# Optimization experiments

Hardware: AMD Instinct MI355X
Metric: run time of the kernel (lower is better)

Reference implementation:

```python
import jax, jax.numpy as jnp
import numpy as np
import math

EMBED = 768
HEADS = 12
DK = EMBED // HEADS
FFN = 3072
NQ = 8
B, S = 4, 2048


def _layernorm(x, g, b, eps=1e-5):
    mu = jnp.mean(x, axis=-1, keepdims=True)
    var = jnp.var(x, axis=-1, keepdims=True)
    return (x - mu) * jax.lax.rsqrt(var + eps) * g + b


def setup_inputs() -> dict:
    key = jax.random.key(0)
    ks = jax.random.split(key, 16)
    std = 0.02
    inp = {
        "x": jax.random.normal(ks[0], (B, S, EMBED), dtype=jnp.float32),
        "mask": jnp.ones((B, S), dtype=jnp.int32),
        # attention projections (torch Linear: W [out, in])
        "wq": jax.random.normal(ks[1], (EMBED, EMBED), jnp.float32) * std,
        "bq": jnp.zeros((EMBED,), jnp.float32),
        "wk": jax.random.normal(ks[2], (EMBED, EMBED), jnp.float32) * std,
        "bk": jnp.zeros((EMBED,), jnp.float32),
        "wv": jax.random.normal(ks[3], (EMBED, EMBED), jnp.float32) * std,
        "bv": jnp.zeros((EMBED,), jnp.float32),
        "wo": jax.random.normal(ks[4], (EMBED, EMBED), jnp.float32) * std,
        "bo": jnp.zeros((EMBED,), jnp.float32),
        # layernorms
        "g1": jnp.ones((EMBED,), jnp.float32),
        "be1": jnp.zeros((EMBED,), jnp.float32),
        "g2": jnp.ones((EMBED,), jnp.float32),
        "be2": jnp.zeros((EMBED,), jnp.float32),
        # quantum FFN: trainable RY angles + two linears
        "theta": jax.random.normal(ks[5], (NQ,), jnp.float32) * 0.1,
        "w1": jax.random.normal(ks[6], (FFN, NQ), jnp.float32) * std,
        "b1": jnp.zeros((FFN,), jnp.float32),
        "w2": jax.random.normal(ks[7], (EMBED, FFN), jnp.float32) * std,
        "b2": jnp.zeros((EMBED,), jnp.float32),
    }
    return inp


def _block(x, mask, wq, bq, wk, bk, wv, bv, wo, bo, g1, be1, g2, be2,
           theta, w1, b1, w2, b2):
    b, s, _ = x.shape
    # --- multi-head attention (dropout = identity at eval) ---
    q = (x @ wq.T + bq).reshape(b, s, HEADS, DK)
    k = (x @ wk.T + bk).reshape(b, s, HEADS, DK)
    v = (x @ wv.T + bv).reshape(b, s, HEADS, DK)
    scores = jnp.einsum("bqhd,bkhd->bhqk", q, k) / math.sqrt(DK)
    scores = jnp.where(mask[:, None, None, :] == 0, -1e9, scores)
    attn = jax.nn.softmax(scores, axis=-1)
    ctx = jnp.einsum("bhqk,bkhd->bqhd", attn, v).reshape(b, s, EMBED)
    attn_out = ctx @ wo.T + bo
    x = _layernorm(x + attn_out, g1, be1)
    # --- quantum FFN: RY(x_i) then RY(theta_i) on |0>, <Z> = cos(x_i+theta_i)
    # (product state, no entanglement -> exact closed form, fully batched)
    meas = jnp.cos(x[..., :NQ] + theta)            # [b, s, NQ]
    h = jax.nn.relu(meas @ w1.T + b1)              # [b, s, FFN]
    ffn_out = h @ w2.T + b2                        # [b, s, EMBED]
    return _layernorm(x + ffn_out, g2, be2)


def reference(x, mask, wq, bq, wk, bk, wv, bv, wo, bo, g1, be1, g2, be2,
              theta, w1, b1, w2, b2):
    return _block(x, mask, wq, bq, wk, bk, wv, bv, wo, bo,
                  g1, be1, g2, be2, theta, w1, b1, w2, b2)
```

## Files before the change

### kernel.cpp

```cpp
#include <hip/hip_runtime.h>
#include <hip/hip_bf16.h>


typedef __bf16 bf16_t;
typedef bf16_t bf16x4 __attribute__((ext_vector_type(4)));
typedef bf16_t bf16x8 __attribute__((ext_vector_type(8)));
typedef float floatx4 __attribute__((ext_vector_type(4)));

#define LOG2E 1.44269504088896f

__device__ __forceinline__ void gload16(const bf16_t* g, bf16_t* l) {
    __builtin_amdgcn_global_load_lds(
        (const __attribute__((address_space(1))) unsigned int*)g,
        (__attribute__((address_space(3))) unsigned int*)l,
        16, 0, 0);
}

__global__ __launch_bounds__(256)
void prep(const float* __restrict__ x,
          const float* __restrict__ wq, const float* __restrict__ wk,
          const float* __restrict__ wv, const float* __restrict__ wo,
          const float* __restrict__ w2,
          const float* __restrict__ bq, const float* __restrict__ bk,
          const float* __restrict__ bv,
          bf16_t* __restrict__ xb, bf16_t* __restrict__ wqkv,
          bf16_t* __restrict__ wob, bf16_t* __restrict__ w2b,
          float* __restrict__ bqkv)
{
    const int seg = blockIdx.y;
    const int idx = blockIdx.x * 256 + threadIdx.x;
    if (seg == 0) {
        if (idx >= 1572864) return;
        const float4 f = ((const float4*)x)[idx];
        bf16x4 o = {(bf16_t)f.x, (bf16_t)f.y, (bf16_t)f.z, (bf16_t)f.w};
        ((bf16x4*)xb)[idx] = o;
    } else if (seg == 1) {
        if (idx >= 442368) return;
        const int e = idx * 4;
        const float4 f = (e < 589824) ? ((const float4*)wq)[idx]
                       : (e < 1179648) ? ((const float4*)wk)[idx - 147456]
                                       : ((const float4*)wv)[idx - 294912];
        bf16x4 o = {(bf16_t)f.x, (bf16_t)f.y, (bf16_t)f.z, (bf16_t)f.w};
        ((bf16x4*)wqkv)[idx] = o;
    } else if (seg == 2) {
        if (idx >= 147456) return;
        const float4 f = ((const float4*)wo)[idx];
        bf16x4 o = {(bf16_t)f.x, (bf16_t)f.y, (bf16_t)f.z, (bf16_t)f.w};
        ((bf16x4*)wob)[idx] = o;
    } else if (seg == 3) {
        if (idx >= 589824) return;
        const float4 f = ((const float4*)w2)[idx];
        bf16x4 o = {(bf16_t)f.x, (bf16_t)f.y, (bf16_t)f.z, (bf16_t)f.w};
        ((bf16x4*)w2b)[idx] = o;
    } else {
        if (idx >= 576) return;
        const int e = idx * 4;
        const float4 f = (e < 768) ? ((const float4*)bq)[idx]
                       : (e < 1536) ? ((const float4*)bk)[idx - 192]
                                    : ((const float4*)bv)[idx - 384];
        ((float4*)bqkv)[idx] = f;
    }
}

template<typename TC>
__global__ __launch_bounds__(256)
void gemm_bb(const bf16_t* __restrict__ A, const bf16_t* __restrict__ W,
             const float* __restrict__ bias, TC* __restrict__ C,
             int kPer, int lda, int ldw, int ldc, int splitStride)
{
    __shared__ __align__(16) bf16_t As[4096];
    __shared__ __align__(16) bf16_t Bs[4096];
    const int tid  = threadIdx.x;
    const int wave = tid >> 6;
    const int lane = tid & 63;
    const int wm = (wave >> 1) * 64;
    const int wn = (wave & 1) * 64;
    const int bm = blockIdx.y * 128;
    const int bn = blockIdx.x * 128;
    const int fr = lane & 15;
    const int fk = (lane >> 4) * 8;

    const int kBeg = blockIdx.z * kPer;
    const int kEnd = kBeg + kPer;
    C += (size_t)blockIdx.z * splitStride;

    const int srow = tid >> 2;
    const int scol = (tid & 3) * 8;
    bf16_t* lA = &As[tid * 8];
    bf16_t* lB = &Bs[tid * 8];

    floatx4 acc[4][4] = {};

    for (int k0 = kBeg; k0 < kEnd; k0 += 32) {
        const bf16_t* ga = A + (size_t)(bm + srow) * lda + k0 + scol;
        const bf16_t* gb = W + (size_t)(bn + srow) * ldw + k0 + scol;
        gload16(ga,                     lA);
        gload16(ga + (size_t)64 * lda,  lA + 2048);
        gload16(gb,                     lB);
        gload16(gb + (size_t)64 * ldw,  lB + 2048);
        __syncthreads();

        bf16x8 fa[4], fb[4];
        #pragma unroll
        for (int i = 0; i < 4; ++i) {
            fa[i] = *(const bf16x8*)&As[(wm + i * 16 + fr) * 32 + fk];
            fb[i] = *(const bf16x8*)&Bs[(wn + i * 16 + fr) * 32 + fk];
        }
        #pragma unroll
        for (int mi = 0; mi < 4; ++mi)
            #pragma unroll
            for (int ni = 0; ni < 4; ++ni)
                acc[mi][ni] = __builtin_amdgcn_mfma_f32_16x16x32_bf16(
                    fa[mi], fb[ni], acc[mi][ni], 0, 0, 0);
        __syncthreads();
    }

    const int fg = (lane >> 4) * 4;
    const bool addb = (blockIdx.z == 0);
    #pragma unroll
    for (int mi = 0; mi < 4; ++mi) {
        #pragma unroll
        for (int ni = 0; ni < 4; ++ni) {
            const int col = bn + wn + ni * 16 + fr;
            const float bv = addb ? bias[col] : 0.f;
            #pragma unroll
            for (int r = 0; r < 4; ++r) {
                const int row = bm + wm + mi * 16 + fg + r;
                C[(size_t)row * ldc + col] = (TC)(acc[mi][ni][r] + bv);
            }
        }
    }
}

__global__ __launch_bounds__(256)
void attn_mfma(const bf16_t* __restrict__ qkv, const int* __restrict__ mask,
               bf16_t* __restrict__ ctx)
{
    __shared__ bf16_t Ks[64][72];
    __shared__ bf16_t Vt[80][72];
    __shared__ float  mb_s[64];
    __shared__ bf16_t Pl[4][32][72];

    const int bh = blockIdx.y;
    const int b = bh / 12, h = bh % 12;
    const int tid  = threadIdx.x;
    const int wave = tid >> 6;
    const int lane = tid & 63;
    const int g    = lane >> 4;
    const int fr   = lane & 15;
    const int qbase = blockIdx.x * 128 + wave * 32;

    for (int idx = tid; idx < 16 * 72; idx += 256) {
        const int rr = idx / 72, cc = idx % 72;
        Vt[64 + rr][cc] = (bf16_t)(rr == 0 ? 1.f : 0.f);
    }

    bf16x8 qf[2][2];
    #pragma unroll
    for (int qt = 0; qt < 2; ++qt)
        #pragma unroll
        for (int s = 0; s < 2; ++s) {
            const size_t tok = (size_t)(b * 2048 + qbase + qt * 16 + fr);
            qf[qt][s] = *(const bf16x8*)(qkv + tok * 2304 + h * 64 + s * 32 + g * 8);
            #pragma unroll
            for (int j = 0; j < 8; ++j)
                qf[qt][s][j] = (bf16_t)((float)qf[qt][s][j] * 0.125f);
        }

    floatx4 o[2][4] = {};
    floatx4 oe[2] = {};

    const int skey = tid & 63;
    const int sgrp = tid >> 6;

    for (int kt = 0; kt < 32; ++kt) {
        __syncthreads();
        {
            const size_t ktok = (size_t)(b * 2048 + kt * 64 + skey) * 2304 + h * 64;
            const bf16x8 k0 = *(const bf16x8*)(qkv + ktok + 768 + sgrp * 16);
            const bf16x8 k1 = *(const bf16x8*)(qkv + ktok + 768 + sgrp * 16 + 8);
            *(bf16x8*)&Ks[skey][sgrp * 16]     = k0;
            *(bf16x8*)&Ks[skey][sgrp * 16 + 8] = k1;
            const bf16x8 v0 = *(const bf16x8*)(qkv + ktok + 1536 + sgrp * 16);
            const bf16x8 v1 = *(const bf16x8*)(qkv + ktok + 1536 + sgrp * 16 + 8);
            #pragma unroll
            for (int j = 0; j < 8; ++j) {
                Vt[sgrp * 16 + j][skey]     = v0[j];
                Vt[sgrp * 16 + 8 + j][skey] = v1[j];
            }
            if (tid < 64)
                mb_s[tid] = (mask[b * 2048 + kt * 64 + tid] == 0) ? -1e9f : 0.f;
        }
        __syncthreads();

        floatx4 st_[2][4] = {};
        #pragma unroll
        for (int s = 0; s < 2; ++s) {
            bf16x8 kf[4];
            #pragma unroll
            for (int ct = 0; ct < 4; ++ct)
                kf[ct] = *(const bf16x8*)&Ks[ct * 16 + fr][s * 32 + g * 8];
            #pragma unroll
            for (int qt = 0; qt < 2; ++qt)
                #pragma unroll
                for (int ct = 0; ct < 4; ++ct)
                    st_[qt][ct] = __builtin_amdgcn_mfma_f32_16x16x32_bf16(
                        kf[ct], qf[qt][s], st_[qt][ct], 0, 0, 0);
        }

        #pragma unroll
        for (int qt = 0; qt < 2; ++qt) {
            #pragma unroll
            for (int ct = 0; ct < 4; ++ct) {
                const float4 mb4 = *(const float4*)&mb_s[ct * 16 + g * 4];
                const float mbr[4] = { mb4.x, mb4.y, mb4.z, mb4.w };
                bf16x4 pw;
                #pragma unroll
                for (int r = 0; r < 4; ++r)
                    pw[r] = (bf16_t)__builtin_amdgcn_exp2f(
                        fmaf(st_[qt][ct][r], LOG2E, mbr[r]));
                *(bf16x4*)&Pl[wave][qt * 16 + fr][ct * 16 + g * 4] = pw;
            }
        }

        #pragma unroll
        for (int st2 = 0; st2 < 2; ++st2) {
            bf16x8 pf[2];
            #pragma unroll
            for (int qt = 0; qt < 2; ++qt)
                pf[qt] = *(const bf16x8*)&Pl[wave][qt * 16 + fr][st2 * 32 + g * 8];
            #pragma unroll
            for (int dt = 0; dt < 4; ++dt) {
                const bf16x8 vf = *(const bf16x8*)&Vt[dt * 16 + fr][st2 * 32 + g * 8];
                #pragma unroll
                for (int qt = 0; qt < 2; ++qt)
                    o[qt][dt] = __builtin_amdgcn_mfma_f32_16x16x32_bf16(
                        pf[qt], vf, o[qt][dt], 0, 0, 0);
            }
            const bf16x8 vo = *(const bf16x8*)&Vt[64 + fr][st2 * 32 + g * 8];
            #pragma unroll
            for (int qt = 0; qt < 2; ++qt)
                oe[qt] = __builtin_amdgcn_mfma_f32_16x16x32_bf16(
                    pf[qt], vo, oe[qt], 0, 0, 0);
        }
    }

    #pragma unroll
    for (int qt = 0; qt < 2; ++qt) {
        float inv[4];
        #pragma unroll
        for (int r = 0; r < 4; ++r) {
            const float lv = __shfl(oe[qt][r], (lane & 48), 64);
            inv[r] = 1.f / lv;
        }
        #pragma unroll
        for (int dt = 0; dt < 4; ++dt)
            #pragma unroll
            for (int r = 0; r < 4; ++r) {
                const size_t row = (size_t)(b * 2048 + qbase + qt * 16 + g * 4 + r);
                ctx[row * 768 + h * 64 + dt * 16 + fr] = (bf16_t)(o[qt][dt][r] * inv[r]);
            }
    }
}

__global__ __launch_bounds__(256)
void ln_fuse(const float* __restrict__ xin, const float* __restrict__ proj,
             const float* __restrict__ proj2,
             const float* __restrict__ g, const float* __restrict__ be,
             float* __restrict__ out,
             const float* __restrict__ theta, float* __restrict__ meas)
{
    const int row = blockIdx.x;
    const int tid = threadIdx.x;
    const size_t base = (size_t)row * 768;
    float v0 = xin[base + tid]       + proj[base + tid];
    float v1 = xin[base + tid + 256] + proj[base + tid + 256];
    float v2 = xin[base + tid + 512] + proj[base + tid + 512];
    if (proj2 != nullptr) {
        v0 += proj2[base + tid];
        v1 += proj2[base + tid + 256];
        v2 += proj2[base + tid + 512];
    }
    float s1 = v0 + v1 + v2;
    float s2 = v0*v0 + v1*v1 + v2*v2;
    #pragma unroll
    for (int mk = 32; mk >= 1; mk >>= 1) {
        s1 += __shfl_xor(s1, mk, 64);
        s2 += __shfl_xor(s2, mk, 64);
    }
    __shared__ float w1s[4], w2s[4];
    const int wave = tid >> 6;
    if ((tid & 63) == 0) { w1s[wave] = s1; w2s[wave] = s2; }
    __syncthreads();
    const float tot1 = w1s[0] + w1s[1] + w1s[2] + w1s[3];
    const float tot2 = w2s[0] + w2s[1] + w2s[2] + w2s[3];
    const float mu   = tot1 * (1.f / 768.f);
    const float var  = tot2 * (1.f / 768.f) - mu * mu;
    const float rinv = rsqrtf(var + 1e-5f);
    const float y0 = (v0 - mu) * rinv * g[tid] + be[tid];
    out[base + tid]       = y0;
    out[base + tid + 256] = (v1 - mu) * rinv * g[tid + 256] + be[tid + 256];
    out[base + tid + 512] = (v2 - mu) * rinv * g[tid + 512] + be[tid + 512];
    if (meas != nullptr && tid < 8)
        meas[row * 8 + tid] = cosf(y0 + theta[tid]);
}

__global__ __launch_bounds__(256)
void ffn1(const float* __restrict__ meas, const float* __restrict__ w1,
          const float* __restrict__ b1, bf16_t* __restrict__ h)
{
    const int row = blockIdx.x;
    __shared__ float ms[8];
    if (threadIdx.x < 8) ms[threadIdx.x] = meas[row * 8 + threadIdx.x];
    __syncthreads();
    #pragma unroll
    for (int i = 0; i < 12; ++i) {
        const int f = threadIdx.x + i * 256;
        const float4 wa = *(const float4*)(w1 + f * 8);
        const float4 wb = *(const float4*)(w1 + f * 8 + 4);
        float v = b1[f];
        v += ms[0]*wa.x + ms[1]*wa.y + ms[2]*wa.z + ms[3]*wa.w;
        v += ms[4]*wb.x + ms[5]*wb.y + ms[6]*wb.z + ms[7]*wb.w;
        h[(size_t)row * 3072 + f] = (bf16_t)fmaxf(v, 0.f);
    }
}

extern "C" void kernel_launch(void* const* d_in, const int* in_sizes, int n_in,
                              void* d_out, int out_size, void* d_ws, size_t ws_size,
                              hipStream_t stream)
{
    const float* x     = (const float*)d_in[0];
    const int*   mask  = (const int*)d_in[1];
    const float* wq    = (const float*)d_in[2];
    const float* bq    = (const float*)d_in[3];
    const float* wk    = (const float*)d_in[4];
    const float* bk    = (const float*)d_in[5];
    const float* wv    = (const float*)d_in[6];
    const float* bv    = (const float*)d_in[7];
    const float* wo    = (const float*)d_in[8];
    const float* bo    = (const float*)d_in[9];
    const float* g1    = (const float*)d_in[10];
    const float* be1   = (const float*)d_in[11];
    const float* g2    = (const float*)d_in[12];
    const float* be2   = (const float*)d_in[13];
    const float* theta = (const float*)d_in[14];
    const float* w1    = (const float*)d_in[15];
    const float* b1    = (const float*)d_in[16];
    const float* w2    = (const float*)d_in[17];
    const float* b2    = (const float*)d_in[18];
    float* out = (float*)d_out;

    char* ws = (char*)d_ws;
    bf16_t* qkv    = (bf16_t*)(ws + 0);
    bf16_t* ctx    = (bf16_t*)(ws + 37748736);
    float*  attnp  = (float*)(ws + 50331648);
    float*  y      = (float*)(ws + 100663296);
    float*  meas   = (float*)(ws + 125829120);
    bf16_t* xb     = (bf16_t*)(ws + 126091264);
    bf16_t* wqkv   = (bf16_t*)(ws + 138674176);
    bf16_t* wob    = (bf16_t*)(ws + 142213120);
    bf16_t* w2b    = (bf16_t*)(ws + 143392768);
    float*  bqkv   = (float*)(ws + 148111360);
    float*  ffnp   = (float*)(ws + 0);
    bf16_t* h      = (bf16_t*)(ws + 50331648);

    const dim3 blk(256);

    prep<<<dim3(6144, 5), blk, 0, stream>>>(x, wq, wk, wv, wo, w2, bq, bk, bv,
                                            xb, wqkv, wob, w2b, bqkv);

    gemm_bb<bf16_t><<<dim3(18, 64, 1), blk, 0, stream>>>(
        xb, wqkv, bqkv, qkv, 768, 768, 768, 2304, 0);

    attn_mfma<<<dim3(16, 48), blk, 0, stream>>>(qkv, mask, ctx);

    gemm_bb<float><<<dim3(6, 64, 2), blk, 0, stream>>>(
        ctx, wob, bo, attnp, 384, 768, 768, 768, 6291456);

    ln_fuse<<<dim3(8192), blk, 0, stream>>>(x, attnp, attnp + 6291456,
                                            g1, be1, y, theta, meas);

    ffn1<<<dim3(8192), blk, 0, stream>>>(meas, w1, b1, h);

    gemm_bb<float><<<dim3(6, 64, 2), blk, 0, stream>>>(
        h, w2b, b2, ffnp, 1536, 3072, 3072, 768, 6291456);

    ln_fuse<<<dim3(8192), blk, 0, stream>>>(y, ffnp, ffnp + 6291456,
                                            g2, be2, out, nullptr, nullptr);
}
```

Before: 319.9 us.

## Double-buffer GEMM loads, swizzle block order, prefetch attention KV, wave-per-row layernorm

The GEMM now double-buffers its LDS tiles so the next k-slice's global-to-LDS load overlaps the current MFMA work, and it remaps block indices to change L2 locality. Attention prefetches the next K/V tile into registers, uses a swizzled 1-D grid, and drops the per-query 0.125 scaling by folding that scale into Wq and bq during prep. Layernorm switches to one wave per row with float4 accesses and no LDS reduction. The GEMM's double buffer doubles LDS use per block, which may reduce occupancy.

```diff
diff --git a/kernel.cpp b/kernel.cpp
--- a/kernel.cpp
+++ b/kernel.cpp
@@ -37,9 +37,10 @@
     } else if (seg == 1) {
         if (idx >= 442368) return;
         const int e = idx * 4;
-        const float4 f = (e < 589824) ? ((const float4*)wq)[idx]
-                       : (e < 1179648) ? ((const float4*)wk)[idx - 147456]
-                                       : ((const float4*)wv)[idx - 294912];
+        float4 f = (e < 589824) ? ((const float4*)wq)[idx]
+                 : (e < 1179648) ? ((const float4*)wk)[idx - 147456]
+                                 : ((const float4*)wv)[idx - 294912];
+        if (e < 589824) { f.x *= 0.125f; f.y *= 0.125f; f.z *= 0.125f; f.w *= 0.125f; }
         bf16x4 o = {(bf16_t)f.x, (bf16_t)f.y, (bf16_t)f.z, (bf16_t)f.w};
         ((bf16x4*)wqkv)[idx] = o;
     } else if (seg == 2) {
@@ -55,9 +56,10 @@
     } else {
         if (idx >= 576) return;
         const int e = idx * 4;
-        const float4 f = (e < 768) ? ((const float4*)bq)[idx]
-                       : (e < 1536) ? ((const float4*)bk)[idx - 192]
-                                    : ((const float4*)bv)[idx - 384];
+        float4 f = (e < 768) ? ((const float4*)bq)[idx]
+                 : (e < 1536) ? ((const float4*)bk)[idx - 192]
+                              : ((const float4*)bv)[idx - 384];
+        if (e < 768) { f.x *= 0.125f; f.y *= 0.125f; f.z *= 0.125f; f.w *= 0.125f; }
         ((float4*)bqkv)[idx] = f;
     }
 }
@@ -68,15 +70,20 @@
              const float* __restrict__ bias, TC* __restrict__ C,
              int kPer, int lda, int ldw, int ldc, int splitStride)
 {
-    __shared__ __align__(16) bf16_t As[4096];
-    __shared__ __align__(16) bf16_t Bs[4096];
+    __shared__ __align__(16) bf16_t As[2][4096];
+    __shared__ __align__(16) bf16_t Bs[2][4096];
     const int tid  = threadIdx.x;
     const int wave = tid >> 6;
     const int lane = tid & 63;
     const int wm = (wave >> 1) * 64;
     const int wn = (wave & 1) * 64;
-    const int bm = blockIdx.y * 128;
-    const int bn = blockIdx.x * 128;
+
+    const int nwg  = gridDim.x * gridDim.y;
+    const int flat = blockIdx.y * gridDim.x + blockIdx.x;
+    const int swz  = (flat & 7) * (nwg >> 3) + (flat >> 3);
+    const int bm = (swz / gridDim.x) * 128;
+    const int bn = (swz % gridDim.x) * 128;
+
     const int fr = lane & 15;
     const int fk = (lane >> 4) * 8;
 
@@ -86,25 +93,33 @@
 
     const int srow = tid >> 2;
     const int scol = (tid & 3) * 8;
-    bf16_t* lA = &As[tid * 8];
-    bf16_t* lB = &Bs[tid * 8];
 
     floatx4 acc[4][4] = {};
 
+    const bf16_t* gA = A + (size_t)(bm + srow) * lda + scol;
+    const bf16_t* gB = W + (size_t)(bn + srow) * ldw + scol;
+
+#define STAGE(buf, kk)                                              \
+    {   const bf16_t* ga = gA + (kk);                               \
+        const bf16_t* gb = gB + (kk);                               \
+        gload16(ga,                    &As[buf][tid * 8]);          \
+        gload16(ga + (size_t)64 * lda, &As[buf][tid * 8 + 2048]);   \
+        gload16(gb,                    &Bs[buf][tid * 8]);          \
+        gload16(gb + (size_t)64 * ldw, &Bs[buf][tid * 8 + 2048]);   \
+    }
+
+    STAGE(0, kBeg);
+    __syncthreads();
+
+    int cur = 0;
     for (int k0 = kBeg; k0 < kEnd; k0 += 32) {
-        const bf16_t* ga = A + (size_t)(bm + srow) * lda + k0 + scol;
-        const bf16_t* gb = W + (size_t)(bn + srow) * ldw + k0 + scol;
-        gload16(ga,                     lA);
-        gload16(ga + (size_t)64 * lda,  lA + 2048);
-        gload16(gb,                     lB);
-        gload16(gb + (size_t)64 * ldw,  lB + 2048);
-        __syncthreads();
+        if (k0 + 32 < kEnd) STAGE(cur ^ 1, k0 + 32);
 
         bf16x8 fa[4], fb[4];
         #pragma unroll
         for (int i = 0; i < 4; ++i) {
-            fa[i] = *(const bf16x8*)&As[(wm + i * 16 + fr) * 32 + fk];
-            fb[i] = *(const bf16x8*)&Bs[(wn + i * 16 + fr) * 32 + fk];
+            fa[i] = *(const bf16x8*)&As[cur][(wm + i * 16 + fr) * 32 + fk];
+            fb[i] = *(const bf16x8*)&Bs[cur][(wn + i * 16 + fr) * 32 + fk];
         }
         #pragma unroll
         for (int mi = 0; mi < 4; ++mi)
@@ -112,8 +127,11 @@
             for (int ni = 0; ni < 4; ++ni)
                 acc[mi][ni] = __builtin_amdgcn_mfma_f32_16x16x32_bf16(
                     fa[mi], fb[ni], acc[mi][ni], 0, 0, 0);
+
         __syncthreads();
-    }
+        cur ^= 1;
+    }
+#undef STAGE
 
     const int fg = (lane >> 4) * 4;
     const bool addb = (blockIdx.z == 0);
@@ -141,14 +159,16 @@
     __shared__ float  mb_s[64];
     __shared__ bf16_t Pl[4][32][72];
 
-    const int bh = blockIdx.y;
+    const int flat = blockIdx.x;
+    const int swz  = (flat & 7) * 96 + (flat >> 3);
+    const int bh = swz >> 4;
     const int b = bh / 12, h = bh % 12;
     const int tid  = threadIdx.x;
     const int wave = tid >> 6;
     const int lane = tid & 63;
     const int g    = lane >> 4;
     const int fr   = lane & 15;
-    const int qbase = blockIdx.x * 128 + wave * 32;
+    const int qbase = (swz & 15) * 128 + wave * 32;
 
     for (int idx = tid; idx < 16 * 72; idx += 256) {
         const int rr = idx / 72, cc = idx % 72;
@@ -162,9 +182,6 @@
         for (int s = 0; s < 2; ++s) {
             const size_t tok = (size_t)(b * 2048 + qbase + qt * 16 + fr);
             qf[qt][s] = *(const bf16x8*)(qkv + tok * 2304 + h * 64 + s * 32 + g * 8);
-            #pragma unroll
-            for (int j = 0; j < 8; ++j)
-                qf[qt][s][j] = (bf16_t)((float)qf[qt][s][j] * 0.125f);
         }
 
     floatx4 o[2][4] = {};
@@ -173,25 +190,37 @@
     const int skey = tid & 63;
     const int sgrp = tid >> 6;
 
+    bf16x8 rk0, rk1, rv0, rv1;
+    float  rmb;
+    {
+        const size_t ktok = (size_t)(b * 2048 + skey) * 2304 + h * 64;
+        rk0 = *(const bf16x8*)(qkv + ktok + 768 + sgrp * 16);
+        rk1 = *(const bf16x8*)(qkv + ktok + 768 + sgrp * 16 + 8);
+        rv0 = *(const bf16x8*)(qkv + ktok + 1536 + sgrp * 16);
+        rv1 = *(const bf16x8*)(qkv + ktok + 1536 + sgrp * 16 + 8);
+        rmb = (mask[b * 2048 + skey] == 0) ? -1e9f : 0.f;
+    }
+
     for (int kt = 0; kt < 32; ++kt) {
         __syncthreads();
-        {
-            const size_t ktok = (size_t)(b * 2048 + kt * 64 + skey) * 2304 + h * 64;
-            const bf16x8 k0 = *(const bf16x8*)(qkv + ktok + 768 + sgrp * 16);
-            const bf16x8 k1 = *(const bf16x8*)(qkv + ktok + 768 + sgrp * 16 + 8);
-            *(bf16x8*)&Ks[skey][sgrp * 16]     = k0;
-            *(bf16x8*)&Ks[skey][sgrp * 16 + 8] = k1;
-            const bf16x8 v0 = *(const bf16x8*)(qkv + ktok + 1536 + sgrp * 16);
-            const bf16x8 v1 = *(const bf16x8*)(qkv + ktok + 1536 + sgrp * 16 + 8);
-            #pragma unroll
-            for (int j = 0; j < 8; ++j) {
-                Vt[sgrp * 16 + j][skey]     = v0[j];
-                Vt[sgrp * 16 + 8 + j][skey] = v1[j];
-            }
-            if (tid < 64)
-                mb_s[tid] = (mask[b * 2048 + kt * 64 + tid] == 0) ? -1e9f : 0.f;
-        }
+        *(bf16x8*)&Ks[skey][sgrp * 16]     = rk0;
+        *(bf16x8*)&Ks[skey][sgrp * 16 + 8] = rk1;
+        #pragma unroll
+        for (int j = 0; j < 8; ++j) {
+            Vt[sgrp * 16 + j][skey]     = rv0[j];
+            Vt[sgrp * 16 + 8 + j][skey] = rv1[j];
+        }
+        if (tid < 64) mb_s[tid] = rmb;
         __syncthreads();
+
+        if (kt + 1 < 32) {
+            const size_t ktok = (size_t)(b * 2048 + (kt + 1) * 64 + skey) * 2304 + h * 64;
+            rk0 = *(const bf16x8*)(qkv + ktok + 768 + sgrp * 16);
+            rk1 = *(const bf16x8*)(qkv + ktok + 768 + sgrp * 16 + 8);
+            rv0 = *(const bf16x8*)(qkv + ktok + 1536 + sgrp * 16);
+            rv1 = *(const bf16x8*)(qkv + ktok + 1536 + sgrp * 16 + 8);
+            rmb = (mask[b * 2048 + (kt + 1) * 64 + skey] == 0) ? -1e9f : 0.f;
+        }
 
         floatx4 st_[2][4] = {};
         #pragma unroll
@@ -270,39 +299,53 @@
              float* __restrict__ out,
              const float* __restrict__ theta, float* __restrict__ meas)
 {
-    const int row = blockIdx.x;
-    const int tid = threadIdx.x;
+    const int wave = threadIdx.x >> 6;
+    const int lane = threadIdx.x & 63;
+    const int row  = blockIdx.x * 4 + wave;
     const size_t base = (size_t)row * 768;
-    float v0 = xin[base + tid]       + proj[base + tid];
-    float v1 = xin[base + tid + 256] + proj[base + tid + 256];
-    float v2 = xin[base + tid + 512] + proj[base + tid + 512];
-    if (proj2 != nullptr) {
-        v0 += proj2[base + tid];
-        v1 += proj2[base + tid + 256];
-        v2 += proj2[base + tid + 512];
-    }
-    float s1 = v0 + v1 + v2;
-    float s2 = v0*v0 + v1*v1 + v2*v2;
+
+    float4 v[3];
+    float s1 = 0.f, s2 = 0.f;
+    #pragma unroll
+    for (int i = 0; i < 3; ++i) {
+        const int c4 = lane + i * 64;
+        const float4 a  = ((const float4*)(xin  + base))[c4];
+        const float4 p  = ((const float4*)(proj + base))[c4];
+        const float4 p2 = ((const float4*)(proj2 + base))[c4];
+        v[i].x = a.x + p.x + p2.x;
+        v[i].y = a.y + p.y + p2.y;
+        v[i].z = a.z + p.z + p2.z;
+        v[i].w = a.w + p.w + p2.w;
+        s1 += v[i].x + v[i].y + v[i].z + v[i].w;
+        s2 += v[i].x*v[i].x + v[i].y*v[i].y + v[i].z*v[i].z + v[i].w*v[i].w;
+    }
     #pragma unroll
     for (int mk = 32; mk >= 1; mk >>= 1) {
         s1 += __shfl_xor(s1, mk, 64);
         s2 += __shfl_xor(s2, mk, 64);
     }
-    __shared__ float w1s[4], w2s[4];
-    const int wave = tid >> 6;
-    if ((tid & 63) == 0) { w1s[wave] = s1; w2s[wave] = s2; }
-    __syncthreads();
-    const float tot1 = w1s[0] + w1s[1] + w1s[2] + w1s[3];
-    const float tot2 = w2s[0] + w2s[1] + w2s[2] + w2s[3];
-    const float mu   = tot1 * (1.f / 768.f);
-    const float var  = tot2 * (1.f / 768.f) - mu * mu;
+    const float mu   = s1 * (1.f / 768.f);
+    const float var  = s2 * (1.f / 768.f) - mu * mu;
     const float rinv = rsqrtf(var + 1e-5f);
-    const float y0 = (v0 - mu) * rinv * g[tid] + be[tid];
-    out[base + tid]       = y0;
-    out[base + tid + 256] = (v1 - mu) * rinv * g[tid + 256] + be[tid + 256];
-    out[base + tid + 512] = (v2 - mu) * rinv * g[tid + 512] + be[tid + 512];
-    if (meas != nullptr && tid < 8)
-        meas[row * 8 + tid] = cosf(y0 + theta[tid]);
+
+    #pragma unroll
+    for (int i = 0; i < 3; ++i) {
+        const int c4 = lane + i * 64;
+        const float4 gg = ((const float4*)g)[c4];
+        const float4 bb = ((const float4*)be)[c4];
+        float4 o;
+        o.x = (v[i].x - mu) * rinv * gg.x + bb.x;
+        o.y = (v[i].y - mu) * rinv * gg.y + bb.y;
+        o.z = (v[i].z - mu) * rinv * gg.z + bb.z;
+        o.w = (v[i].w - mu) * rinv * gg.w + bb.w;
+        ((float4*)(out + base))[c4] = o;
+        if (i == 0 && meas != nullptr && lane < 2) {
+            meas[row * 8 + lane * 4 + 0] = cosf(o.x + theta[lane * 4 + 0]);
+            meas[row * 8 + lane * 4 + 1] = cosf(o.y + theta[lane * 4 + 1]);
+            meas[row * 8 + lane * 4 + 2] = cosf(o.z + theta[lane * 4 + 2]);
+            meas[row * 8 + lane * 4 + 3] = cosf(o.w + theta[lane * 4 + 3]);
+        }
+    }
 }
 
 __global__ __launch_bounds__(256)
@@ -372,12 +415,12 @@
     gemm_bb<bf16_t><<<dim3(18, 64, 1), blk, 0, stream>>>(
         xb, wqkv, bqkv, qkv, 768, 768, 768, 2304, 0);
 
-    attn_mfma<<<dim3(16, 48), blk, 0, stream>>>(qkv, mask, ctx);
+    attn_mfma<<<dim3(768), blk, 0, stream>>>(qkv, mask, ctx);
 
     gemm_bb<float><<<dim3(6, 64, 2), blk, 0, stream>>>(
         ctx, wob, bo, attnp, 384, 768, 768, 768, 6291456);
 
-    ln_fuse<<<dim3(8192), blk, 0, stream>>>(x, attnp, attnp + 6291456,
+    ln_fuse<<<dim3(2048), blk, 0, stream>>>(x, attnp, attnp + 6291456,
                                             g1, be1, y, theta, meas);
 
     ffn1<<<dim3(8192), blk, 0, stream>>>(meas, w1, b1, h);
@@ -385,6 +428,6 @@
     gemm_bb<float><<<dim3(6, 64, 2), blk, 0, stream>>>(
         h, w2b, b2, ffnp, 1536, 3072, 3072, 768, 6291456);
 
-    ln_fuse<<<dim3(8192), blk, 0, stream>>>(y, ffnp, ffnp + 6291456,
+    ln_fuse<<<dim3(2048), blk, 0, stream>>>(y, ffnp, ffnp + 6291456,
                                             g2, be2, out, nullptr, nullptr);
 }
```

New measurement: 293.0 us. 8.4% less time.
